# Performance work log

Measured on AMD Instinct MI355X. Metric: run time of the kernel, lower is better.

The kernel has to match this reference:

```python
import math
import jax, jax.numpy as jnp
from jax import lax
import numpy as np

N = 512          # transform size; frame size = 2N
B = 16           # batch
T = 2048         # number of frames; signal length = N*T
PI = math.pi


def _make_mdct_filter(n: int, normalize: bool = True) -> jnp.ndarray:
    # filter[k, 0, t] = cos(pi/N * (t + 0.5 + N/2) * (k + 0.5)) / sqrt(N)
    k = jnp.arange(n, dtype=jnp.float32).reshape(n, 1, 1)
    t = jnp.arange(2 * n, dtype=jnp.float32).reshape(1, 1, 2 * n)
    f = jnp.cos(PI / n * (t + 0.5 + n / 2) * (k + 0.5))
    if normalize:
        f = f / jnp.sqrt(jnp.float32(n))
    return f  # [N, 1, 2N]


def setup_inputs() -> dict:
    key = jax.random.key(0)
    x = jax.random.normal(key, (B, 1, N * T), dtype=jnp.float32)
    mdct_filter = _make_mdct_filter(N, normalize=True)
    return {"x": x, "mdct_filter": mdct_filter}


def reference(x, mdct_filter):
    # Equivalent of F.conv1d(x, filter, stride=N, padding=N)
    n = mdct_filter.shape[0]
    # x: [B, 1, N*T] -> out: [B, N, T+1]
    out = lax.conv_general_dilated(
        x, mdct_filter,
        window_strides=(n,),
        padding=[(n, n)],
        dimension_numbers=("NCH", "OIH", "NCH"),
    )
    return out
```

## Files before the change

kernel.cpp:

```cpp
#include <hip/hip_runtime.h>
#include <hip/hip_bf16.h>
#include <stdint.h>
#include <stddef.h>


constexpr int N_ = 512;
constexpr int T_ = 2048;
constexpr int B_ = 16;
constexpr int LEN = N_ * T_;
constexpr int FRAMES = T_ + 1;
constexpr int COLS = B_ * FRAMES;
constexpr int NT_TILES = 257;
constexpr int COLS_PAD = NT_TILES * 128;
constexpr int KF = 512;
constexpr int BK = 64;
constexpr int TILE_H = 128 * BK;

typedef __attribute__((ext_vector_type(8))) _Float16 f16x8;
typedef __attribute__((ext_vector_type(4))) _Float16 f16x4;
typedef __attribute__((ext_vector_type(4))) float f32x4;

#define GLD16(gptr, lptr)                                                     \
  __builtin_amdgcn_global_load_lds(                                           \
      (const __attribute__((address_space(1))) unsigned int*)(gptr),          \
      (__attribute__((address_space(3))) unsigned int*)(lptr), 16, 0, 0)

__global__ void prep_filter(const float* __restrict__ f,
                            _Float16* __restrict__ D) {
  int idx = (blockIdx.x * 256 + threadIdx.x) * 4;
  int k = idx >> 9;
  int j = idx & 511;
  int t = (j < 256) ? j : (j + 256);
  const float4 v = *(const float4*)&f[k * 1024 + t];
  f16x4 h = {(_Float16)v.x, (_Float16)v.y, (_Float16)v.z, (_Float16)v.w};
  *(f16x4*)&D[k * KF + j] = h;
}

__global__ void fold_x(const float* __restrict__ x, _Float16* __restrict__ V) {
  const int blk = (blockIdx.x & 7) * 1028 + (blockIdx.x >> 3);
  const int c = blk * 4 + (threadIdx.x >> 6);
  const int l = threadIdx.x & 63;
  const bool mi = (l < 32);
  const int j0 = mi ? (l * 8) : (256 + (l - 32) * 8);
  const float sgn = mi ? -1.0f : 1.0f;
  float4 a0 = {0.f, 0.f, 0.f, 0.f}, a1 = {0.f, 0.f, 0.f, 0.f};
  float4 r0 = {0.f, 0.f, 0.f, 0.f}, r1 = {0.f, 0.f, 0.f, 0.f};
  if (c < COLS) {
    int b = (int)((unsigned)c / (unsigned)FRAMES);
    int o = c - b * FRAMES;
    const int lo = b * LEN;
    const int g = lo + o * N_ - N_;
    const int fb = g + (mi ? j0 : (j0 + 256));
    const int rb = g + (mi ? (504 - j0) : (1272 - j0));
    if ((unsigned)(fb - lo) <= (unsigned)(LEN - 8)) {
      a0 = *(const float4*)(x + fb);
      a1 = *(const float4*)(x + fb + 4);
    }
    if ((unsigned)(rb - lo) <= (unsigned)(LEN - 8)) {
      r0 = *(const float4*)(x + rb);
      r1 = *(const float4*)(x + rb + 4);
    }
  }
  f16x8 h;
  h[0] = (_Float16)__builtin_fmaf(sgn, r1.w, a0.x);
  h[1] = (_Float16)__builtin_fmaf(sgn, r1.z, a0.y);
  h[2] = (_Float16)__builtin_fmaf(sgn, r1.y, a0.z);
  h[3] = (_Float16)__builtin_fmaf(sgn, r1.x, a0.w);
  h[4] = (_Float16)__builtin_fmaf(sgn, r0.w, a1.x);
  h[5] = (_Float16)__builtin_fmaf(sgn, r0.z, a1.y);
  h[6] = (_Float16)__builtin_fmaf(sgn, r0.y, a1.z);
  h[7] = (_Float16)__builtin_fmaf(sgn, r0.x, a1.w);
  if (c < COLS_PAD) *(f16x8*)&V[(size_t)c * KF + j0] = h;
}

__global__ __launch_bounds__(256, 2) void gemm_fold(
    const _Float16* __restrict__ D, const _Float16* __restrict__ V,
    float* __restrict__ out) {
  __shared__ __align__(16) _Float16 SMEM[4 * TILE_H];
  _Float16* const As0 = SMEM;
  _Float16* const Bs0 = SMEM + TILE_H;
  _Float16* const As1 = SMEM + 2 * TILE_H;
  _Float16* const Bs1 = SMEM + 3 * TILE_H;

  const int id = blockIdx.x;
  const int xcd = id & 7;
  const int sb = id >> 3;
  const int nt = (sb >> 2) * 8 + xcd;
  if (nt >= NT_TILES) return;
  const int m0 = (sb & 3) * 128;
  const int n0 = nt * 128;

  if ((id >> 8) & 1) {
    __builtin_amdgcn_s_sleep(15);
  }

  const int tid = threadIdx.x;
  const int wid = tid >> 6;
  const int lane = tid & 63;
  const int quad = lane >> 4;
  const int l16 = lane & 15;
  const int mw = (wid >> 1) * 64;
  const int nw = (wid & 1) * 64;

  f32x4 acc[4][4];
#pragma unroll
  for (int i = 0; i < 4; ++i)
#pragma unroll
    for (int j = 0; j < 4; ++j) acc[i][j] = (f32x4){0.f, 0.f, 0.f, 0.f};

#define STAGE(AS, BS, KT)                                                     \
  do {                                                                        \
    const int kb_ = (KT) * BK;                                                \
    _Pragma("unroll")                                                         \
    for (int it = 0; it < 4; ++it) {                                          \
      const int S_ = it * 256 + tid;      \
      const int r_ = S_ >> 3;                                   \
      const int c_ = (S_ & 7) ^ (r_ & 7);          \
      const int g_ = kb_ + c_ * 8;                                            \
      GLD16(D + (size_t)(m0 + r_) * KF + g_, &(AS)[S_ * 8]);                  \
      GLD16(V + (size_t)(n0 + r_) * KF + g_, &(BS)[S_ * 8]);                  \
    }                                                                         \
  } while (0)

#define COMPUTE(AS, BS)                                                       \
  do {                                                                        \
    _Pragma("unroll")                                                         \
    for (int ko = 0; ko < 2; ++ko) {                                          \
      f16x8 af[4], bf[4];                                                     \
      _Pragma("unroll")                                                       \
      for (int i = 0; i < 4; ++i) {                                           \
        int ra_ = mw + i * 16 + l16;                                          \
        int rb_ = nw + i * 16 + l16;                                          \
        int ca_ = ko * 4 + quad;                                              \
        af[i] = *(const f16x8*)&(AS)[(ra_ * 8 + (ca_ ^ (ra_ & 7))) * 8];      \
        bf[i] = *(const f16x8*)&(BS)[(rb_ * 8 + (ca_ ^ (rb_ & 7))) * 8];      \
      }                                                                       \
      _Pragma("unroll")                                                       \
      for (int i = 0; i < 4; ++i)                                             \
        _Pragma("unroll")                                                     \
        for (int j = 0; j < 4; ++j)                                           \
          acc[i][j] = __builtin_amdgcn_mfma_f32_16x16x32_f16(af[i], bf[j],    \
                                                             acc[i][j],      \
                                                             0, 0, 0);        \
    }                                                                         \
  } while (0)

#define WAITV(N) asm volatile("s_waitcnt vmcnt(" #N ")" ::: "memory")
#define BAR() __builtin_amdgcn_s_barrier()
#define SCHED0() __builtin_amdgcn_sched_barrier(0)

  STAGE(As0, Bs0, 0);

#define STEP(AScur, BScur, ASnxt, BSnxt, KT)                                  \
  do {                                                                        \
    if ((KT) < 7) {                                                           \
      STAGE(ASnxt, BSnxt, (KT) + 1);                                          \
      WAITV(8);                                                               \
    } else {                                                                  \
      WAITV(0);                                                               \
    }                                                                         \
    BAR();                              \
    SCHED0();                                                                 \
    COMPUTE(AScur, BScur);                                                    \
    SCHED0();                                                                 \
    BAR();                     \
  } while (0)

  STEP(As0, Bs0, As1, Bs1, 0);
  STEP(As1, Bs1, As0, Bs0, 1);
  STEP(As0, Bs0, As1, Bs1, 2);
  STEP(As1, Bs1, As0, Bs0, 3);
  STEP(As0, Bs0, As1, Bs1, 4);
  STEP(As1, Bs1, As0, Bs0, 5);
  STEP(As0, Bs0, As1, Bs1, 6);
  STEP(As1, Bs1, As0, Bs0, 7);

#undef STEP
#undef STAGE
#undef COMPUTE
#undef WAITV
#undef BAR
#undef SCHED0

  const int bs = n0 / FRAMES;
  const int os = n0 - bs * FRAMES;
  const bool fast = (os + 128 <= FRAMES) && (n0 + 128 <= COLS);

  if (fast) {
    float* Ct = (float*)SMEM;
#pragma unroll
    for (int i = 0; i < 4; ++i) {
#pragma unroll
      for (int j = 0; j < 4; ++j) {
        const int Lr0 = mw + i * 16 + quad * 4;
        const int Lc = nw + j * 16 + l16;
#pragma unroll
        for (int r = 0; r < 4; ++r) {
          const int row = Lr0 + r;
          Ct[row * 128 + (Lc ^ ((row & 12) << 2))] = acc[i][j][r];
        }
      }
    }
    __syncthreads();
    float* const obase = out + (size_t)bs * N_ * FRAMES + os;
#pragma unroll 4
    for (int it2 = 0; it2 < 32; ++it2) {
      const int row = wid * 32 + it2;
      const int sw = (row & 12) << 2;
      const int grow = m0 + row;
      const float v0 = Ct[row * 128 + (lane ^ sw)];
      const float v1 = Ct[row * 128 + ((64 + lane) ^ sw)];
      float* rp = obase + (size_t)grow * FRAMES;
      rp[lane] = v0;
      rp[64 + lane] = v1;
    }
  } else {
#pragma unroll
    for (int i = 0; i < 4; ++i) {
#pragma unroll
      for (int j = 0; j < 4; ++j) {
        int col = n0 + nw + j * 16 + l16;
        if (col < COLS) {
          int b = col / FRAMES;
          int o = col - b * FRAMES;
          int rowb = m0 + mw + i * 16 + quad * 4;
          float* op = out + (size_t)b * N_ * FRAMES + (size_t)rowb * FRAMES + o;
#pragma unroll
          for (int r = 0; r < 4; ++r) op[(size_t)r * FRAMES] = acc[i][j][r];
        }
      }
    }
  }
}

__global__ void naive_conv(const float* __restrict__ x, const float* __restrict__ f,
                           float* __restrict__ out) {
  int col = blockIdx.x;
  int k = threadIdx.x;
  __shared__ float win[1024];
  int b = col / FRAMES;
  int o = col - b * FRAMES;
  const float* xb = x + (size_t)b * LEN;
  int g = o * N_ - N_;
  for (int t = threadIdx.x; t < 1024; t += 512) {
    int i = g + t;
    win[t] = (i >= 0 && i < LEN) ? xb[i] : 0.0f;
  }
  __syncthreads();
  float s = 0.0f;
  const float* fk = f + (size_t)k * 1024;
  for (int t = 0; t < 1024; ++t) s += win[t] * fk[t];
  out[(size_t)b * N_ * FRAMES + (size_t)k * FRAMES + o] = s;
}

extern "C" void kernel_launch(void* const* d_in, const int* in_sizes, int n_in,
                              void* d_out, int out_size, void* d_ws, size_t ws_size,
                              hipStream_t stream) {
  const float* x = (const float*)d_in[0];
  const float* f = (const float*)d_in[1];
  float* out = (float*)d_out;

  const size_t elems_D = (size_t)512 * 512;
  const size_t elems_V = (size_t)COLS_PAD * KF;
  const size_t need = (elems_D + elems_V) * sizeof(_Float16);

  if (ws_size < need) {
    naive_conv<<<COLS, 512, 0, stream>>>(x, f, out);
    return;
  }

  _Float16* D = (_Float16*)d_ws;
  _Float16* V = D + elems_D;

  prep_filter<<<256, 256, 0, stream>>>(f, D);
  fold_x<<<COLS_PAD / 4, 256, 0, stream>>>(x, V);
  gemm_fold<<<1056, 256, 0, stream>>>(D, V, out);
}
```

Baseline: 140.8 us.

## Load GEMM A operand directly into registers, staging only B through LDS

The DCT-matrix operand (D) is no longer copied into shared memory. Each wave now loads its A fragments straight from global memory into double-buffered registers, one k-step ahead. Only the V tile goes through LDS, and one of the two barriers per k-step is dropped. This aims to cut LDS traffic and synchronisation in the main loop. The cost is redundant per-wave global/L2 reads of D and about 64 extra VGPRs for the register double buffer.

```diff
diff --git a/kernel.cpp b/kernel.cpp
--- a/kernel.cpp
+++ b/kernel.cpp
@@ -77,10 +77,8 @@
     const _Float16* __restrict__ D, const _Float16* __restrict__ V,
     float* __restrict__ out) {
   __shared__ __align__(16) _Float16 SMEM[4 * TILE_H];
-  _Float16* const As0 = SMEM;
-  _Float16* const Bs0 = SMEM + TILE_H;
-  _Float16* const As1 = SMEM + 2 * TILE_H;
-  _Float16* const Bs1 = SMEM + 3 * TILE_H;
+  _Float16* const Bs0 = SMEM;
+  _Float16* const Bs1 = SMEM + TILE_H;
 
   const int id = blockIdx.x;
   const int xcd = id & 7;
@@ -102,85 +100,97 @@
   const int mw = (wid >> 1) * 64;
   const int nw = (wid & 1) * 64;
 
+  const _Float16* const Dp = D + (size_t)(m0 + mw + l16) * KF + quad * 8;
+
+  f16x8 ar0[4][2], ar1[4][2];
   f32x4 acc[4][4];
 #pragma unroll
   for (int i = 0; i < 4; ++i)
 #pragma unroll
     for (int j = 0; j < 4; ++j) acc[i][j] = (f32x4){0.f, 0.f, 0.f, 0.f};
 
-#define STAGE(AS, BS, KT)                                                     \
+#define WAITV(N) asm volatile("s_waitcnt vmcnt(" #N ")" ::: "memory")
+#define BAR() __builtin_amdgcn_s_barrier()
+#define SCHED0() __builtin_amdgcn_sched_barrier(0)
+
+#define BSTAGE(BS, KT)                                                        \
   do {                                                                        \
     const int kb_ = (KT) * BK;                                                \
     _Pragma("unroll")                                                         \
     for (int it = 0; it < 4; ++it) {                                          \
-      const int S_ = it * 256 + tid;      \
-      const int r_ = S_ >> 3;                                   \
-      const int c_ = (S_ & 7) ^ (r_ & 7);          \
-      const int g_ = kb_ + c_ * 8;                                            \
-      GLD16(D + (size_t)(m0 + r_) * KF + g_, &(AS)[S_ * 8]);                  \
-      GLD16(V + (size_t)(n0 + r_) * KF + g_, &(BS)[S_ * 8]);                  \
+      const int S_ = it * 256 + tid;                                          \
+      const int r_ = S_ >> 3;                                                 \
+      const int c_ = (S_ & 7) ^ (r_ & 7);                                     \
+      GLD16(V + (size_t)(n0 + r_) * KF + kb_ + c_ * 8, &(BS)[S_ * 8]);        \
     }                                                                         \
   } while (0)
 
-#define COMPUTE(AS, BS)                                                       \
+#define ALOAD(AR, KT)                                                         \
+  do {                                                                        \
+    _Pragma("unroll")                                                         \
+    for (int i = 0; i < 4; ++i)                                               \
+      _Pragma("unroll")                                                       \
+      for (int ko = 0; ko < 2; ++ko)                                          \
+        (AR)[i][ko] = *(const f16x8*)&Dp[(size_t)i * 16 * KF + ko * 32 +      \
+                                         (KT) * 64];                          \
+  } while (0)
+
+#define COMPUTE(BS, AR)                                                       \
   do {                                                                        \
     _Pragma("unroll")                                                         \
     for (int ko = 0; ko < 2; ++ko) {                                          \
-      f16x8 af[4], bf[4];                                                     \
+      f16x8 bf[4];                                                            \
       _Pragma("unroll")                                                       \
       for (int i = 0; i < 4; ++i) {                                           \
-        int ra_ = mw + i * 16 + l16;                                          \
         int rb_ = nw + i * 16 + l16;                                          \
         int ca_ = ko * 4 + quad;                                              \
-        af[i] = *(const f16x8*)&(AS)[(ra_ * 8 + (ca_ ^ (ra_ & 7))) * 8];      \
         bf[i] = *(const f16x8*)&(BS)[(rb_ * 8 + (ca_ ^ (rb_ & 7))) * 8];      \
       }                                                                       \
       _Pragma("unroll")                                                       \
       for (int i = 0; i < 4; ++i)                                             \
         _Pragma("unroll")                                                     \
         for (int j = 0; j < 4; ++j)                                           \
-          acc[i][j] = __builtin_amdgcn_mfma_f32_16x16x32_f16(af[i], bf[j],    \
+          acc[i][j] = __builtin_amdgcn_mfma_f32_16x16x32_f16((AR)[i][ko],     \
+                                                             bf[j],          \
                                                              acc[i][j],      \
                                                              0, 0, 0);        \
     }                                                                         \
   } while (0)
 
-#define WAITV(N) asm volatile("s_waitcnt vmcnt(" #N ")" ::: "memory")
-#define BAR() __builtin_amdgcn_s_barrier()
-#define SCHED0() __builtin_amdgcn_sched_barrier(0)
-
-  STAGE(As0, Bs0, 0);
-
-#define STEP(AScur, BScur, ASnxt, BSnxt, KT)                                  \
-  do {                                                                        \
-    if ((KT) < 7) {                                                           \
-      STAGE(ASnxt, BSnxt, (KT) + 1);                                          \
-      WAITV(8);                                                               \
-    } else {                                                                  \
-      WAITV(0);                                                               \
-    }                                                                         \
-    BAR();                              \
+#define STEP(BSc, BSn, ARc, ARn, KT)                                          \
+  do {                                                                        \
+    BSTAGE(BSn, (KT) + 1);                                                    \
+    ALOAD(ARn, (KT) + 1);                                                     \
+    WAITV(12);                                                                \
     SCHED0();                                                                 \
-    COMPUTE(AScur, BScur);                                                    \
+    COMPUTE(BSc, ARc);                                                        \
     SCHED0();                                                                 \
-    BAR();                     \
-  } while (0)
-
-  STEP(As0, Bs0, As1, Bs1, 0);
-  STEP(As1, Bs1, As0, Bs0, 1);
-  STEP(As0, Bs0, As1, Bs1, 2);
-  STEP(As1, Bs1, As0, Bs0, 3);
-  STEP(As0, Bs0, As1, Bs1, 4);
-  STEP(As1, Bs1, As0, Bs0, 5);
-  STEP(As0, Bs0, As1, Bs1, 6);
-  STEP(As1, Bs1, As0, Bs0, 7);
+    WAITV(8);                                                                 \
+    BAR();                                                                    \
+  } while (0)
+
+  BSTAGE(Bs0, 0);
+  ALOAD(ar0, 0);
+  WAITV(8);
+  BAR();
+
+  STEP(Bs0, Bs1, ar0, ar1, 0);
+  STEP(Bs1, Bs0, ar1, ar0, 1);
+  STEP(Bs0, Bs1, ar0, ar1, 2);
+  STEP(Bs1, Bs0, ar1, ar0, 3);
+  STEP(Bs0, Bs1, ar0, ar1, 4);
+  STEP(Bs1, Bs0, ar1, ar0, 5);
+  STEP(Bs0, Bs1, ar0, ar1, 6);
+  WAITV(0);
+  SCHED0();
+  COMPUTE(Bs1, ar1);
+  SCHED0();
+  BAR();
 
 #undef STEP
-#undef STAGE
 #undef COMPUTE
-#undef WAITV
-#undef BAR
-#undef SCHED0
+#undef ALOAD
+#undef BSTAGE
 
   const int bs = n0 / FRAMES;
   const int os = n0 - bs * FRAMES;
@@ -231,6 +241,9 @@
       }
     }
   }
+#undef WAITV
+#undef BAR
+#undef SCHED0
 }
 
 __global__ void naive_conv(const float* __restrict__ x, const float* __restrict__ f,
```

After: 164.5 us. 1.17x slower.
